# Optimization experiments

Hardware: AMD Instinct MI355X
Metric: run time of the kernel (lower is better)

Reference implementation:

```python
import jax, jax.numpy as jnp
import numpy as np

N = 100000
E = 1600000
D = 128


def _sage_conv(x, src, dst, W_l, W_r, b):
    # PyG SAGEConv (aggr='mean', project=False, root_weight=True):
    #   out = lin_l(mean_{j in N(i)} x_j) + lin_r(x_i), bias lives in lin_l.
    msg = x[src]                                            # [E, D] gather
    s = jax.ops.segment_sum(msg, dst, num_segments=N)       # [N, D]
    cnt = jax.ops.segment_sum(jnp.ones((src.shape[0],), x.dtype), dst, num_segments=N)
    mean = s / jnp.maximum(cnt, 1.0)[:, None]               # mean aggregation
    return mean @ W_l.T + x @ W_r.T + b


def setup_inputs() -> dict:
    key = jax.random.key(0)
    ks = jax.random.split(key, 8)
    x = jax.random.normal(ks[0], (N, D), dtype=jnp.float32)
    edge_index = jax.random.randint(ks[1], (2, E), 0, N, dtype=jnp.int64)
    scale = 1.0 / np.sqrt(D)
    params = {}
    for i, k in enumerate(ks[2:8]):
        pass
    W_l1 = jax.random.uniform(ks[2], (D, D), jnp.float32, -scale, scale)
    W_r1 = jax.random.uniform(ks[3], (D, D), jnp.float32, -scale, scale)
    W_l2 = jax.random.uniform(ks[4], (D, D), jnp.float32, -scale, scale)
    W_r2 = jax.random.uniform(ks[5], (D, D), jnp.float32, -scale, scale)
    W_l3 = jax.random.uniform(ks[6], (D, D), jnp.float32, -scale, scale)
    W_r3 = jax.random.uniform(ks[7], (D, D), jnp.float32, -scale, scale)
    b1 = jnp.zeros((D,), jnp.float32)
    b2 = jnp.zeros((D,), jnp.float32)
    b3 = jnp.zeros((D,), jnp.float32)
    return {"x": x, "edge_index": edge_index,
            "W_l1": W_l1, "W_r1": W_r1, "b1": b1,
            "W_l2": W_l2, "W_r2": W_r2, "b2": b2,
            "W_l3": W_l3, "W_r3": W_r3, "b3": b3}


def reference(x, edge_index, W_l1, W_r1, b1, W_l2, W_r2, b2, W_l3, W_r3, b3):
    src, dst = edge_index[0], edge_index[1]
    h = jax.nn.relu(_sage_conv(x, src, dst, W_l1, W_r1, b1))
    h = jax.nn.relu(_sage_conv(h, src, dst, W_l2, W_r2, b2))
    h = _sage_conv(h, src, dst, W_l3, W_r3, b3)
    return h
```

## Files before the change

### kernel.cpp

```cpp
#include <hip/hip_runtime.h>


typedef __bf16 bf16x8 __attribute__((ext_vector_type(8)));
typedef float  f32x4  __attribute__((ext_vector_type(4)));

#define DFEAT 128
#define PAD 64
#define PITCH 136
#define BSH 7
#define BNODES 128
#define CAP_PB 40
#define CHUNK 8192
#define NBMAX 1024

__device__ __forceinline__ unsigned int pack_bf16x2(float2 v) {
    unsigned int lo = (unsigned int)__builtin_bit_cast(unsigned short, (__bf16)v.x);
    unsigned int hi = (unsigned int)__builtin_bit_cast(unsigned short, (__bf16)v.y);
    return lo | (hi << 16);
}

struct WPtrs  { const float* s[6]; };
struct WBPtrs { unsigned int* d[6]; };

__global__ __launch_bounds__(256) void k_pass1(const int* __restrict__ src,
                                               const int* __restrict__ dst, int E,
                                               int nb, int eblk,
                                               int* __restrict__ cnt,
                                               unsigned int* __restrict__ binned2,
                                               const float* __restrict__ x,
                                               uint2* __restrict__ xb4,
                                               int xw4, int xblk,
                                               WPtrs ws, WBPtrs wd) {
    __shared__ int cnt2[NBMAX];
    int b = blockIdx.x;
    int t = threadIdx.x;
    if (b < eblk) {
        for (int i = t; i < nb; i += 256) cnt2[i] = 0;
        __syncthreads();
        int base4 = (b * CHUNK) >> 2;
        const int4* d4p = (const int4*)dst;
        const int4* s4p = (const int4*)src;
        int e4max = E >> 2;
#pragma unroll
        for (int hb = 0; hb < 2; ++hb) {
            int4 dv[4], sv[4];
#pragma unroll
            for (int j = 0; j < 4; ++j) {
                int i4 = base4 + (hb * 4 + j) * 256 + t;
                bool ok = (i4 < e4max);
                int i4c = ok ? i4 : 0;
                dv[j] = d4p[i4c];
                sv[j] = s4p[i4c];
                if (!ok) dv[j] = make_int4(-1, -1, -1, -1);
            }
            int r[16];
#pragma unroll
            for (int j = 0; j < 4; ++j) {
                int dd[4] = {dv[j].x, dv[j].y, dv[j].z, dv[j].w};
#pragma unroll
                for (int k2 = 0; k2 < 4; ++k2) {
                    int d = dd[k2];
                    r[j * 4 + k2] = (d >= 0) ? atomicAdd(&cnt2[d >> BSH], 1)
                                             : CAP_PB;
                }
            }
#pragma unroll
            for (int j = 0; j < 4; ++j) {
                int dd[4] = {dv[j].x, dv[j].y, dv[j].z, dv[j].w};
                int ss[4] = {sv[j].x, sv[j].y, sv[j].z, sv[j].w};
#pragma unroll
                for (int k2 = 0; k2 < 4; ++k2) {
                    int d = dd[k2];
                    int rr = r[j * 4 + k2];
                    if (d >= 0 && rr < CAP_PB) {
                        binned2[((size_t)(d >> BSH) * eblk + b) * CAP_PB + rr] =
                            (unsigned)ss[k2] |
                            ((unsigned)(d & (BNODES - 1)) << 20);
                    }
                }
            }
        }
        __syncthreads();
        for (int i = t; i < nb; i += 256)
            cnt[(size_t)i * eblk + b] = cnt2[i];
    } else if (b < eblk + xblk) {
        int i = (b - eblk) * 256 + t;
        if (i < xw4) {
            float4 v = ((const float4*)x)[i];
            uint2 o;
            o.x = pack_bf16x2(make_float2(v.x, v.y));
            o.y = pack_bf16x2(make_float2(v.z, v.w));
            xb4[i] = o;
        }
    } else {
        int r = b - eblk - xblk;
        int which = r >> 5;
        int i = (r & 31) * 256 + t;
        wd.d[which][i] = pack_bf16x2(((const float2*)ws.s[which])[i]);
    }
}

__global__ __launch_bounds__(256) void k_pass2(const int* __restrict__ cnt,
                                               const unsigned int* __restrict__ binned2,
                                               int* __restrict__ csr,
                                               int* __restrict__ deg, int N,
                                               int eblk) {
    __shared__ int lcnt[BNODES];
    __shared__ __align__(16) int lcsr[BNODES * PAD];
    __shared__ int pcnt[256];
    int b = blockIdx.x, t = threadIdx.x;
    if (t < BNODES) lcnt[t] = 0;
    pcnt[t] = (t < eblk) ? min(cnt[(size_t)b * eblk + t], CAP_PB) : 0;
    __syncthreads();

    const uint4* reg4 = (const uint4*)(binned2 + (size_t)b * eblk * CAP_PB);
    const int Q4 = CAP_PB / 4;
    int total4 = eblk * Q4;
    for (int i4 = t; i4 < total4; i4 += 256) {
        int blk = i4 / Q4;
        int s4  = (i4 - blk * Q4) * 4;
        int n   = pcnt[blk];
        if (s4 < n) {
            uint4 v4 = reg4[i4];
            unsigned vv[4] = {v4.x, v4.y, v4.z, v4.w};
#pragma unroll
            for (int j = 0; j < 4; ++j) {
                if (s4 + j < n) {
                    unsigned v = vv[j];
                    int nl = (int)(v >> 20);
                    int s  = (int)(v & 0xFFFFFu);
                    int r = atomicAdd(&lcnt[nl], 1);
                    if (r < PAD) lcsr[(nl << 6) + r] = s;
                }
            }
        }
    }
    __syncthreads();

    int node0 = b << BSH;
    int NL = N - node0;
    if (NL > BNODES) NL = BNODES;
    const uint4* ls4 = (const uint4*)lcsr;
    uint4* cs4 = (uint4*)(csr + ((size_t)node0 << 6));
    int n  = t >> 1;
    int hf = t & 1;
    if (n < NL) {
        int d = min(lcnt[n], PAD);
        int nw = (d + 3) >> 2;
        for (int j = hf; j < nw; j += 2)
            cs4[n * 16 + j] = ls4[n * 16 + j];
        if (hf == 0) deg[node0 + n] = d;
    }
}

__global__ __launch_bounds__(256, 4) void k_layer(const __bf16* __restrict__ h,
                                               const int* __restrict__ deg,
                                               const int* __restrict__ csr,
                                               const __bf16* __restrict__ Wl,
                                               const __bf16* __restrict__ Wr,
                                               const float* __restrict__ bias,
                                               __bf16* __restrict__ outb,
                                               float* __restrict__ outf,
                                               int relu) {
    __shared__ __bf16 sm[2][16][PITCH];
    int tid  = threadIdx.x;
    int wave = tid >> 6;
    int lane = tid & 63;
    int g = lane >> 4;
    int c = lane & 15;
    int t0 = blockIdx.x * 16;
    int node = t0 + (wave << 2) + g;
    int row = (wave << 2) + g;

    const uint4* hp4 = (const uint4*)h;

    *(uint4*)&sm[1][row][c * 8] = hp4[(size_t)node * 16 + c];

    int d = deg[node];
    if (d > PAD) d = PAD;
    float acc[8];
#pragma unroll
    for (int j = 0; j < 8; ++j) acc[j] = 0.0f;

    for (int s0 = 0; s0 < d; s0 += 16) {
        int myedge = (s0 + c < d) ? csr[(node << 6) + s0 + c] : 0;
#pragma unroll
        for (int hb = 0; hb < 2; ++hb) {
            uint4 u[8];
#pragma unroll
            for (int kk = 0; kk < 8; ++kk) {
                int slot = s0 + hb * 8 + kk;
                int s = __shfl(myedge, (g << 4) + hb * 8 + kk, 64);
                if (slot < d) u[kk] = hp4[(size_t)s * 16 + c];
                else          u[kk] = make_uint4(0u, 0u, 0u, 0u);
            }
#pragma unroll
            for (int kk = 0; kk < 8; ++kk) {
                unsigned int w0 = u[kk].x, w1 = u[kk].y, w2 = u[kk].z, w3 = u[kk].w;
                acc[0] += __uint_as_float(w0 << 16);
                acc[1] += __uint_as_float(w0 & 0xffff0000u);
                acc[2] += __uint_as_float(w1 << 16);
                acc[3] += __uint_as_float(w1 & 0xffff0000u);
                acc[4] += __uint_as_float(w2 << 16);
                acc[5] += __uint_as_float(w2 & 0xffff0000u);
                acc[6] += __uint_as_float(w3 << 16);
                acc[7] += __uint_as_float(w3 & 0xffff0000u);
            }
        }
    }
    float iv = (d > 0) ? 1.0f / (float)d : 0.0f;
    uint4 o;
    o.x = pack_bf16x2(make_float2(acc[0] * iv, acc[1] * iv));
    o.y = pack_bf16x2(make_float2(acc[2] * iv, acc[3] * iv));
    o.z = pack_bf16x2(make_float2(acc[4] * iv, acc[5] * iv));
    o.w = pack_bf16x2(make_float2(acc[6] * iv, acc[7] * iv));
    *(uint4*)&sm[0][row][c * 8] = o;

    __syncthreads();

    int m = lane & 15;
    int q = lane >> 4;
    f32x4 accj[2];
    accj[0] = (f32x4){0.f, 0.f, 0.f, 0.f};
    accj[1] = (f32x4){0.f, 0.f, 0.f, 0.f};

#pragma unroll
    for (int half = 0; half < 2; ++half) {
        const __bf16* W = half ? Wr : Wl;
#pragma unroll
        for (int kk = 0; kk < 4; ++kk) {
            int k0 = kk * 32 + q * 8;
            bf16x8 a = *(const bf16x8*)&sm[half][m][k0];
#pragma unroll
            for (int jt = 0; jt < 2; ++jt) {
                int j = wave * 32 + jt * 16 + m;
                bf16x8 wfr = *(const bf16x8*)(W + (size_t)j * DFEAT + k0);
                accj[jt] = __builtin_amdgcn_mfma_f32_16x16x32_bf16(a, wfr,
                                                                   accj[jt], 0, 0, 0);
            }
        }
    }

#pragma unroll
    for (int jt = 0; jt < 2; ++jt) {
        int j = wave * 32 + jt * 16 + m;
        float bv = bias[j];
#pragma unroll
        for (int r = 0; r < 4; ++r) {
            float v = accj[jt][r] + bv;
            if (relu) v = fmaxf(v, 0.0f);
            size_t idx = (size_t)(t0 + q * 4 + r) * DFEAT + j;
            if (outb) outb[idx] = (__bf16)v;
            else      outf[idx] = v;
        }
    }
}

extern "C" void kernel_launch(void* const* d_in, const int* in_sizes, int n_in,
                              void* d_out, int out_size, void* d_ws, size_t ws_size,
                              hipStream_t stream) {
    const int N = in_sizes[0] / DFEAT;
    const int E = in_sizes[1] / 2;

    const float* x   = (const float*)d_in[0];
    const int*   ei  = (const int*)d_in[1];
    const int*   src = ei;
    const int*   dst = ei + E;
    const float* b1  = (const float*)d_in[4];
    const float* b2  = (const float*)d_in[7];
    const float* b3  = (const float*)d_in[10];
    float* out = (float*)d_out;

    char* base = (char*)d_ws;
    size_t off = 0;
    auto alloc = [&](size_t nbytes) -> void* {
        off = (off + 255) & ~(size_t)255;
        void* p = base + off;
        off += nbytes;
        return p;
    };
    const int NB  = (N + BNODES - 1) >> BSH;
    const int EB1 = (E + CHUNK - 1) / CHUNK;
    const size_t FEAT_B = (size_t)N * DFEAT * 2;
    int*    deg = (int*)alloc((size_t)N * 4);
    int*    csr = (int*)alloc((size_t)N * PAD * 4);
    int*    cnt = (int*)alloc((size_t)NB * EB1 * 4);
    __bf16* xb  = (__bf16*)alloc(FEAT_B);
    __bf16* h1b = (__bf16*)alloc(FEAT_B);
    __bf16* h2b = (__bf16*)alloc(FEAT_B);
    __bf16* Wb[6];
    for (int i = 0; i < 6; ++i) Wb[i] = (__bf16*)alloc((size_t)DFEAT * DFEAT * 2);
    (void)ws_size;
    unsigned int* binned2 = (unsigned int*)h2b;

    const int XW4  = N * DFEAT / 4;
    const int XBLK = (XW4 + 255) / 256;
    const int TILE_B = N / 16;

    WPtrs  wsrc = {{(const float*)d_in[2], (const float*)d_in[3],
                    (const float*)d_in[5], (const float*)d_in[6],
                    (const float*)d_in[8], (const float*)d_in[9]}};
    WBPtrs wdst = {{(unsigned int*)Wb[0], (unsigned int*)Wb[1],
                    (unsigned int*)Wb[2], (unsigned int*)Wb[3],
                    (unsigned int*)Wb[4], (unsigned int*)Wb[5]}};

    k_pass1<<<EB1 + XBLK + 6 * 32, 256, 0, stream>>>(src, dst, E, NB, EB1, cnt,
                                                     binned2, x, (uint2*)xb,
                                                     XW4, XBLK, wsrc, wdst);
    k_pass2<<<NB, 256, 0, stream>>>(cnt, binned2, csr, deg, N, EB1);

    k_layer<<<TILE_B, 256, 0, stream>>>(xb,  deg, csr, Wb[0], Wb[1], b1, h1b, nullptr, 1);
    k_layer<<<TILE_B, 256, 0, stream>>>(h1b, deg, csr, Wb[2], Wb[3], b2, h2b, nullptr, 1);
    k_layer<<<TILE_B, 256, 0, stream>>>(h2b, deg, csr, Wb[4], Wb[5], b3, nullptr, out, 0);
}
```

Measured before the change: 392.9 us.

## Split fused gather+GEMM layer kernel into separate gather and GEMM kernels

Each layer previously ran one kernel that both gathered and mean-aggregated neighbour features and ran the MFMA projections. It is now split into a gather kernel with higher occupancy (launch bounds 8), which writes the mean to a bf16 scratch buffer, and a separate GEMM kernel that reads that buffer and the root features. Existing buffers are reused in rotation as scratch. The aim is more waves in flight for the latency-bound gather, at the cost of an extra round trip of the mean matrix through global memory and three more kernel launches.

New measurement: 873.3 us. +122.3%, slower.

```diff
diff --git a/kernel.cpp b/kernel.cpp
--- a/kernel.cpp
+++ b/kernel.cpp
@@ -153,28 +153,18 @@
     }
 }
 
-__global__ __launch_bounds__(256, 4) void k_layer(const __bf16* __restrict__ h,
-                                               const int* __restrict__ deg,
-                                               const int* __restrict__ csr,
-                                               const __bf16* __restrict__ Wl,
-                                               const __bf16* __restrict__ Wr,
-                                               const float* __restrict__ bias,
-                                               __bf16* __restrict__ outb,
-                                               float* __restrict__ outf,
-                                               int relu) {
-    __shared__ __bf16 sm[2][16][PITCH];
+__global__ __launch_bounds__(256, 8) void k_gather(const __bf16* __restrict__ h,
+                                                   const int* __restrict__ deg,
+                                                   const int* __restrict__ csr,
+                                                   __bf16* __restrict__ mb) {
     int tid  = threadIdx.x;
     int wave = tid >> 6;
     int lane = tid & 63;
     int g = lane >> 4;
     int c = lane & 15;
-    int t0 = blockIdx.x * 16;
-    int node = t0 + (wave << 2) + g;
-    int row = (wave << 2) + g;
+    int node = blockIdx.x * 16 + (wave << 2) + g;
 
     const uint4* hp4 = (const uint4*)h;
-
-    *(uint4*)&sm[1][row][c * 8] = hp4[(size_t)node * 16 + c];
 
     int d = deg[node];
     if (d > PAD) d = PAD;
@@ -214,10 +204,31 @@
     o.y = pack_bf16x2(make_float2(acc[2] * iv, acc[3] * iv));
     o.z = pack_bf16x2(make_float2(acc[4] * iv, acc[5] * iv));
     o.w = pack_bf16x2(make_float2(acc[6] * iv, acc[7] * iv));
-    *(uint4*)&sm[0][row][c * 8] = o;
-
+    ((uint4*)mb)[(size_t)node * 16 + c] = o;
+}
+
+__global__ __launch_bounds__(256, 4) void k_gemm(const __bf16* __restrict__ h,
+                                                 const __bf16* __restrict__ mb,
+                                                 const __bf16* __restrict__ Wl,
+                                                 const __bf16* __restrict__ Wr,
+                                                 const float* __restrict__ bias,
+                                                 __bf16* __restrict__ outb,
+                                                 float* __restrict__ outf,
+                                                 int relu) {
+    __shared__ __bf16 sm[2][16][PITCH];
+    int tid  = threadIdx.x;
+    int t0 = blockIdx.x * 16;
+    {
+        int row = tid >> 4;
+        int c16 = tid & 15;
+        size_t gi = (size_t)(t0 + row) * 16 + c16;
+        *(uint4*)&sm[0][row][c16 * 8] = ((const uint4*)mb)[gi];
+        *(uint4*)&sm[1][row][c16 * 8] = ((const uint4*)h)[gi];
+    }
     __syncthreads();
 
+    int wave = tid >> 6;
+    int lane = tid & 63;
     int m = lane & 15;
     int q = lane >> 4;
     f32x4 accj[2];
@@ -309,7 +320,10 @@
                                                      XW4, XBLK, wsrc, wdst);
     k_pass2<<<NB, 256, 0, stream>>>(cnt, binned2, csr, deg, N, EB1);
 
-    k_layer<<<TILE_B, 256, 0, stream>>>(xb,  deg, csr, Wb[0], Wb[1], b1, h1b, nullptr, 1);
-    k_layer<<<TILE_B, 256, 0, stream>>>(h1b, deg, csr, Wb[2], Wb[3], b2, h2b, nullptr, 1);
-    k_layer<<<TILE_B, 256, 0, stream>>>(h2b, deg, csr, Wb[4], Wb[5], b3, nullptr, out, 0);
-}
+    k_gather<<<TILE_B, 256, 0, stream>>>(xb,  deg, csr, h2b);
+    k_gemm<<<TILE_B, 256, 0, stream>>>(xb,  h2b, Wb[0], Wb[1], b1, h1b, nullptr, 1);
+    k_gather<<<TILE_B, 256, 0, stream>>>(h1b, deg, csr, xb);
+    k_gemm<<<TILE_B, 256, 0, stream>>>(h1b, xb,  Wb[2], Wb[3], b2, h2b, nullptr, 1);
+    k_gather<<<TILE_B, 256, 0, stream>>>(h2b, deg, csr, h1b);
+    k_gemm<<<TILE_B, 256, 0, stream>>>(h2b, h1b, Wb[4], Wb[5], b3, nullptr, out, 0);
+}
```
